# Performance work log

Hardware: AMD Instinct MI355X
Metric: run time of the kernel (lower is better)

Reference implementation:

```python
import jax, jax.numpy as jnp
import numpy as np

B, N, F_DIM, M, K, D = 8, 16384, 6, 128, 16, 768
MLP_DIMS = [F_DIM, 256, 512, 768, D]


def _fps(pts):
    """Deterministic farthest point sampling. pts: [N,4] -> indices [M] (first pick = point 0)."""
    n = pts.shape[0]

    def step(carry, _):
        min_d, last = carry
        d = jnp.sum((pts - pts[last]) ** 2, axis=-1)
        min_d = jnp.minimum(min_d, d)
        nxt = jnp.argmax(min_d).astype(jnp.int32)
        return (min_d, nxt), nxt

    init = (jnp.full((n,), 1e30, dtype=pts.dtype), jnp.int32(0))
    _, idx = jax.lax.scan(step, init, None, length=M - 1)
    return jnp.concatenate([jnp.zeros((1,), jnp.int32), idx])


def setup_inputs() -> dict:
    key = jax.random.key(0)
    ks = jax.random.split(key, 16)
    bidx = jnp.repeat(jnp.arange(B, dtype=jnp.float32), N)[:, None]
    xyzt = jax.random.normal(ks[0], (B * N, 4), jnp.float32)
    coordinates = jnp.concatenate([bidx, xyzt], axis=1)  # [B*N, 5]
    features = jax.random.normal(ks[1], (B * N, F_DIM), jnp.float32)
    inp = {"coordinates": coordinates, "features": features}
    for i in range(4):
        di, do = MLP_DIMS[i], MLP_DIMS[i + 1]
        inp[f"W{i}"] = jax.random.normal(ks[2 + i], (di, do), jnp.float32) * np.float32(1.0 / np.sqrt(di))
        inp[f"b{i}"] = jnp.zeros((do,), jnp.float32)
    for j in range(2):
        inp[f"Wn{j}"] = jax.random.normal(ks[6 + j], (D, D), jnp.float32) * np.float32(1.0 / np.sqrt(D))
        inp[f"bn{j}"] = jnp.zeros((D,), jnp.float32)
    return inp


def _forward(coordinates, features, W0, b0, W1, b1, W2, b2, W3, b3, Wn0, bn0, Wn1, bn1):
    # Equal points per event, sorted batch ids -> plain reshape replaces the per-batch loop.
    pts = coordinates.reshape(B, N, 5)[:, :, 1:5]       # xyz + time  [B,N,4]
    h = features.reshape(B, N, F_DIM)
    # per-point MLP (ReLU after each hidden layer, final Linear has no activation)
    h = jax.nn.relu(h @ W0 + b0)
    h = jax.nn.relu(h @ W1 + b1)
    h = jax.nn.relu(h @ W2 + b2)
    pf = h @ W3 + b3                                    # [B,N,D]
    # FPS centroids (non-differentiable index selection, as in the torch/cpu original)
    fidx = jax.vmap(_fps)(jax.lax.stop_gradient(pts))   # [B,M]
    cent = jnp.take_along_axis(pts, fidx[:, :, None], axis=1)  # [B,M,4]
    # cdist + kNN (smallest distances)
    dist = jnp.sqrt(jnp.sum((cent[:, :, None, :] - pts[:, None, :, :]) ** 2, axis=-1))  # [B,M,N]
    _, knn = jax.lax.top_k(-dist, K)                    # [B,M,K]
    gathered = jax.vmap(lambda p, i: p[i])(pf, knn)     # [B,M,K,D]
    pooled = jnp.max(gathered, axis=2)                  # [B,M,D]
    t = jax.nn.relu(pooled @ Wn0 + bn0)
    tokens = t @ Wn1 + bn1                              # [B,M,D]
    # sort tokens/centroids by centroid time (column 3)
    order = jnp.argsort(cent[:, :, 3], axis=1)
    cent = jnp.take_along_axis(cent, order[:, :, None], axis=1)
    tokens = jnp.take_along_axis(tokens, order[:, :, None], axis=1)
    masks = jnp.ones((B, M), dtype=bool)  # num_points > max_tokens -> all tokens valid
    return tokens, cent, masks


def reference(coordinates, features, W0, b0, W1, b1, W2, b2, W3, b3, Wn0, bn0, Wn1, bn1):
    return _forward(coordinates, features, W0, b0, W1, b1, W2, b2, W3, b3, Wn0, bn0, Wn1, bn1)
```

## Files before the change

kernel.cpp:

```cpp
#include <hip/hip_runtime.h>

#define B_ 8
#define N_ 16384
#define F_ 6
#define M_ 128
#define K_ 16
#define D_ 768

typedef unsigned short u16;
typedef unsigned int u32;
typedef __attribute__((ext_vector_type(8))) short short8;
typedef __attribute__((ext_vector_type(4))) float f32x4;
typedef __attribute__((ext_vector_type(2))) float f32x2;

__device__ __forceinline__ u16 f2bf(float f){
  union { float f; u32 i; } v; v.f = f;
  u32 x = v.i;
  u32 r = x + 0x7FFFu + ((x >> 16) & 1u);
  return (u16)(r >> 16);
}

__global__ __launch_bounds__(256) void conv_wt(const float* __restrict__ W,
                                               u16* __restrict__ WT, int K, int N){
  __shared__ u16 tile[64][65];
  int tiles_n = N >> 6;
  int tk = blockIdx.x / tiles_n, tn = blockIdx.x % tiles_n;
  int k0 = tk << 6, n0 = tn << 6;
  int t = threadIdx.x;
#pragma unroll
  for (int q = 0; q < 16; q++){
    int idx = q * 256 + t;
    int kk = idx >> 6, nn = idx & 63;
    tile[kk][nn] = f2bf(W[(size_t)(k0 + kk) * N + n0 + nn]);
  }
  __syncthreads();
#pragma unroll
  for (int q = 0; q < 16; q++){
    int idx = q * 256 + t;
    int nn = idx >> 6, kk = idx & 63;
    WT[(size_t)(n0 + nn) * K + k0 + kk] = tile[kk][nn];
  }
}

#define FPW 16
__global__ __launch_bounds__(512, 2) void fps_kernel(const float* __restrict__ coords,
                                                     float* __restrict__ cent){
#pragma clang fp contract(off)
  __shared__ float s_wv[2][8];
  __shared__ int s_wi[2][8];
  int b = blockIdx.x;
  int t = threadIdx.x;
  const float* cb = coords + (size_t)b * N_ * 5;
  f32x2 px[FPW], py[FPW], pz[FPW], pw[FPW], md[FPW];
#pragma unroll
  for (int j = 0; j < FPW; j++){
    int p = t + (j << 9);
    size_t i0 = (size_t)(2 * p) * 5;
    px[j] = (f32x2){cb[i0+1], cb[i0+6]};
    py[j] = (f32x2){cb[i0+2], cb[i0+7]};
    pz[j] = (f32x2){cb[i0+3], cb[i0+8]};
    pw[j] = (f32x2){cb[i0+4], cb[i0+9]};
    md[j] = (f32x2){1e30f, 1e30f};
  }
  float cx = cb[1], cy = cb[2], cz = cb[3], ct = cb[4];
  if (t == 0){
    float* c0 = cent + (size_t)b * M_ * 4;
    c0[0]=cx; c0[1]=cy; c0[2]=cz; c0[3]=ct;
  }
  for (int step = 1; step < M_; step++){
    f32x2 cx2 = (f32x2){cx, cx}, cy2 = (f32x2){cy, cy};
    f32x2 cz2 = (f32x2){cz, cz}, ct2 = (f32x2){ct, ct};
    float bv = -1.0f; int bi = 1 << 30;
#pragma unroll
    for (int j = 0; j < FPW; j++){
      f32x2 dX = px[j] - cx2;
      f32x2 dY = py[j] - cy2;
      f32x2 s = dX*dX + dY*dY;
      f32x2 dZ = pz[j] - cz2;
      s = s + dZ*dZ;
      f32x2 dW = pw[j] - ct2;
      s = s + dW*dW;
      f32x2 m = md[j];
      m[0] = (s[0] < m[0]) ? s[0] : m[0];
      m[1] = (s[1] < m[1]) ? s[1] : m[1];
      md[j] = m;
      int i0 = (t + (j << 9)) << 1;
      if (m[0] > bv){ bv = m[0]; bi = i0; }
      if (m[1] > bv){ bv = m[1]; bi = i0 + 1; }
    }
#pragma unroll
    for (int off = 32; off > 0; off >>= 1){
      float ov = __shfl_down(bv, off);
      int oi = __shfl_down(bi, off);
      if (ov > bv || (ov == bv && oi < bi)){ bv = ov; bi = oi; }
    }
    int par = step & 1;
    if ((t & 63) == 0){ s_wv[par][t >> 6] = bv; s_wi[par][t >> 6] = bi; }
    __syncthreads();
    float fv = s_wv[par][t & 7];
    int fi = s_wi[par][t & 7];
#pragma unroll
    for (int off = 1; off < 8; off <<= 1){
      float ov = __shfl_xor(fv, off);
      int oi = __shfl_xor(fi, off);
      if (ov > fv || (ov == fv && oi < fi)){ fv = ov; fi = oi; }
    }
    fi &= (N_ - 1);
    size_t wbase = (size_t)fi * 5;
    cx = cb[wbase+1]; cy = cb[wbase+2]; cz = cb[wbase+3]; ct = cb[wbase+4];
    if (t == 0){
      float* cr = cent + ((size_t)b * M_ + step) * 4;
      cr[0]=cx; cr[1]=cy; cr[2]=cz; cr[3]=ct;
    }
  }
}

__global__ __launch_bounds__(128) void rank_scatter(const float* __restrict__ cent_fps,
                                                    float* __restrict__ cent_sorted,
                                                    float* __restrict__ out,
                                                    size_t out_elems){
  int b = blockIdx.x, m = threadIdx.x;
  __shared__ float tt[M_];
  const float* row = cent_fps + ((size_t)b * M_ + m) * 4;
  float x=row[0], y=row[1], z=row[2], w=row[3];
  tt[m] = w;
  __syncthreads();
  int rank = 0;
  for (int j = 0; j < M_; j++){
    float tj = tt[j];
    if (tj < w || (tj == w && j < m)) rank++;
  }
  float* dst = cent_sorted + ((size_t)b * M_ + rank) * 4;
  dst[0]=x; dst[1]=y; dst[2]=z; dst[3]=w;
  size_t co = (size_t)B_ * M_ * D_ + ((size_t)b * M_ + rank) * 4;
  if (co + 3 < out_elems){
    out[co+0]=x; out[co+1]=y; out[co+2]=z; out[co+3]=w;
  }
  size_t mo = (size_t)B_ * M_ * D_ + (size_t)B_ * M_ * 4 + (size_t)b * M_ + m;
  if (mo < out_elems) out[mo] = 1.0f;
}

#define KNT 512
#define KPT 32
__global__ __launch_bounds__(512) void knn_kernel(const float* __restrict__ coords,
                                                  const float* __restrict__ cent,
                                                  int* __restrict__ knn){
#pragma clang fp contract(off)
  int cm = blockIdx.x;
  int b = cm >> 7;
  const float* cb = coords + (size_t)b * N_ * 5;
  int t = threadIdx.x;
  float cx=cent[cm*4+0], cy=cent[cm*4+1], cz=cent[cm*4+2], ct=cent[cm*4+3];
  float dist[KPT];
#pragma unroll
  for (int j = 0; j < KPT; j++){
    size_t i = t + j * KNT;
    float dx=cb[i*5+1]-cx, dy=cb[i*5+2]-cy, dz=cb[i*5+3]-cz, dw=cb[i*5+4]-ct;
    float d = ((dx*dx + dy*dy) + dz*dz) + dw*dw;
    dist[j] = sqrtf(d);
  }
  __shared__ float s_wv[8];
  __shared__ int s_wi[8];
  __shared__ int s_bi;
  for (int r = 0; r < K_; r++){
    float bv = 3e38f; int bi = 1 << 30;
#pragma unroll
    for (int j = 0; j < KPT; j++){
      int i = t + j * KNT;
      float v = dist[j];
      if (v < bv){ bv = v; bi = i; }
    }
#pragma unroll
    for (int off = 32; off > 0; off >>= 1){
      float ov = __shfl_down(bv, off);
      int oi = __shfl_down(bi, off);
      if (ov < bv || (ov == bv && oi < bi)){ bv = ov; bi = oi; }
    }
    if ((t & 63) == 0){ s_wv[t >> 6] = bv; s_wi[t >> 6] = bi; }
    __syncthreads();
    if (t == 0){
      float fv = s_wv[0]; int fi = s_wi[0];
      for (int w = 1; w < 8; w++){
        float wv = s_wv[w]; int wi = s_wi[w];
        if (wv < fv || (wv == fv && wi < fi)){ fv = wv; fi = wi; }
      }
      s_bi = fi;
      knn[(size_t)cm * K_ + r] = fi & (N_ - 1);
    }
    __syncthreads();
    int wi = s_bi;
#pragma unroll
    for (int j = 0; j < KPT; j++){
      if (t + j * KNT == wi) dist[j] = 3e38f;
    }
  }
}

__global__ __launch_bounds__(256) void gather_l0(const float* __restrict__ feat,
                                                 const int* __restrict__ knn,
                                                 const float* __restrict__ W0,
                                                 const float* __restrict__ b0,
                                                 u16* __restrict__ h1,
                                                 int rowBase){
  __shared__ float sW[F_][256];
  __shared__ float sb[256];
  __shared__ float sfa[32][F_];
  int t = threadIdx.x;
#pragma unroll
  for (int k = 0; k < F_; k++) sW[k][t] = W0[k * 256 + t];
  sb[t] = b0[t];
  if (t < 32 * F_){
    int r = t / F_, k = t % F_;
    int grow = rowBase + blockIdx.x * 32 + r;
    int bb = grow >> 11;
    int idx = knn[grow] & (N_ - 1);
    sfa[r][k] = feat[((size_t)bb * N_ + idx) * F_ + k];
  }
  __syncthreads();
#pragma unroll 4
  for (int r = 0; r < 32; r++){
    float acc = sb[t];
#pragma unroll
    for (int k = 0; k < F_; k++) acc = fmaf(sfa[r][k], sW[k][t], acc);
    int lrow = blockIdx.x * 32 + r;
    h1[(size_t)lrow * 256 + t] = f2bf(fmaxf(acc, 0.0f));
  }
}

template<int RELU, int OUTF32>
__global__ __launch_bounds__(256) void gemm_bf16(const u16* __restrict__ A,
                                                 const u16* __restrict__ WT,
                                                 const float* __restrict__ bias,
                                                 void* __restrict__ Cv,
                                                 int Kd, int Nd){
  __shared__ u16 As[128][40];
  __shared__ u16 Bs[128][40];
  const int t = threadIdx.x;
  const int bm = blockIdx.y << 7;
  const int bn = blockIdx.x << 7;
  const int wave = t >> 6;
  const int lane = t & 63;
  const int wm = (wave & 1) << 6;
  const int wn = (wave >> 1) << 6;
  const int lm = lane & 15;
  const int lk = (lane >> 4) << 3;
  f32x4 acc[4][4] = {};
  for (int k0 = 0; k0 < Kd; k0 += 32){
#pragma unroll
    for (int it = 0; it < 2; it++){
      int slot = t + (it << 8);
      int r = slot >> 2;
      int c = (slot & 3) << 3;
      short8 v = *(const short8*)(A + (size_t)(bm + r) * Kd + k0 + c);
      *(short8*)&As[r][c] = v;
      short8 w = *(const short8*)(WT + (size_t)(bn + r) * Kd + k0 + c);
      *(short8*)&Bs[r][c] = w;
    }
    __syncthreads();
    short8 af[4], bfr[4];
#pragma unroll
    for (int mt = 0; mt < 4; mt++) af[mt] = *(const short8*)&As[wm + (mt << 4) + lm][lk];
#pragma unroll
    for (int nt = 0; nt < 4; nt++) bfr[nt] = *(const short8*)&Bs[wn + (nt << 4) + lm][lk];
#pragma unroll
    for (int mt = 0; mt < 4; mt++)
#pragma unroll
      for (int nt = 0; nt < 4; nt++)
        acc[mt][nt] = __builtin_amdgcn_mfma_f32_16x16x32_bf16(af[mt], bfr[nt], acc[mt][nt], 0, 0, 0);
    __syncthreads();
  }
#pragma unroll
  for (int nt = 0; nt < 4; nt++){
    int n = bn + wn + (nt << 4) + lm;
    float bia = bias[n];
#pragma unroll
    for (int mt = 0; mt < 4; mt++){
#pragma unroll
      for (int r2 = 0; r2 < 4; r2++){
        int m = bm + wm + (mt << 4) + ((lane >> 4) << 2) + r2;
        float v = acc[mt][nt][r2] + bia;
        if (RELU) v = fmaxf(v, 0.0f);
        if (OUTF32) ((float*)Cv)[(size_t)m * Nd + n] = v;
        else        ((u16*)Cv)[(size_t)m * Nd + n] = f2bf(v);
      }
    }
  }
}

template<int RELU, int OUTF32>
__global__ __launch_bounds__(256) void gemm64(const u16* __restrict__ A,
                                              const u16* __restrict__ WT,
                                              const float* __restrict__ bias,
                                              void* __restrict__ Cv,
                                              int Kd, int Nd){
  __shared__ u16 As[64][40];
  __shared__ u16 Bs[64][40];
  const int t = threadIdx.x;
  const int bm = blockIdx.y << 6;
  const int bn = blockIdx.x << 6;
  const int wave = t >> 6;
  const int lane = t & 63;
  const int wm = (wave & 1) << 5;
  const int wn = (wave >> 1) << 5;
  const int lm = lane & 15;
  const int lk = (lane >> 4) << 3;
  f32x4 acc[2][2] = {};
  for (int k0 = 0; k0 < Kd; k0 += 32){
    {
      int r = t >> 2;
      int c = (t & 3) << 3;
      short8 v = *(const short8*)(A + (size_t)(bm + r) * Kd + k0 + c);
      *(short8*)&As[r][c] = v;
      short8 w = *(const short8*)(WT + (size_t)(bn + r) * Kd + k0 + c);
      *(short8*)&Bs[r][c] = w;
    }
    __syncthreads();
    short8 af[2], bfr[2];
#pragma unroll
    for (int mt = 0; mt < 2; mt++) af[mt] = *(const short8*)&As[wm + (mt << 4) + lm][lk];
#pragma unroll
    for (int nt = 0; nt < 2; nt++) bfr[nt] = *(const short8*)&Bs[wn + (nt << 4) + lm][lk];
#pragma unroll
    for (int mt = 0; mt < 2; mt++)
#pragma unroll
      for (int nt = 0; nt < 2; nt++)
        acc[mt][nt] = __builtin_amdgcn_mfma_f32_16x16x32_bf16(af[mt], bfr[nt], acc[mt][nt], 0, 0, 0);
    __syncthreads();
  }
#pragma unroll
  for (int nt = 0; nt < 2; nt++){
    int n = bn + wn + (nt << 4) + lm;
    float bia = bias[n];
#pragma unroll
    for (int mt = 0; mt < 2; mt++){
#pragma unroll
      for (int r2 = 0; r2 < 4; r2++){
        int m = bm + wm + (mt << 4) + ((lane >> 4) << 2) + r2;
        float v = acc[mt][nt][r2] + bia;
        if (RELU) v = fmaxf(v, 0.0f);
        if (OUTF32) ((float*)Cv)[(size_t)m * Nd + n] = v;
        else        ((u16*)Cv)[(size_t)m * Nd + n] = f2bf(v);
      }
    }
  }
}

__global__ __launch_bounds__(256) void gemm_pool(const u16* __restrict__ A,
                                                 const u16* __restrict__ WT,
                                                 const float* __restrict__ bias,
                                                 u16* __restrict__ pooled,
                                                 int Kd, int Nd, int groupBase){
  __shared__ u16 As[128][40];
  __shared__ u16 Bs[128][40];
  const int t = threadIdx.x;
  const int bm = blockIdx.y << 7;
  const int bn = blockIdx.x << 7;
  const int wave = t >> 6;
  const int lane = t & 63;
  const int wm = (wave & 1) << 6;
  const int wn = (wave >> 1) << 6;
  const int lm = lane & 15;
  const int lk = (lane >> 4) << 3;
  f32x4 acc[4][4] = {};
  for (int k0 = 0; k0 < Kd; k0 += 32){
#pragma unroll
    for (int it = 0; it < 2; it++){
      int slot = t + (it << 8);
      int r = slot >> 2;
      int c = (slot & 3) << 3;
      short8 v = *(const short8*)(A + (size_t)(bm + r) * Kd + k0 + c);
      *(short8*)&As[r][c] = v;
      short8 w = *(const short8*)(WT + (size_t)(bn + r) * Kd + k0 + c);
      *(short8*)&Bs[r][c] = w;
    }
    __syncthreads();
    short8 af[4], bfr[4];
#pragma unroll
    for (int mt = 0; mt < 4; mt++) af[mt] = *(const short8*)&As[wm + (mt << 4) + lm][lk];
#pragma unroll
    for (int nt = 0; nt < 4; nt++) bfr[nt] = *(const short8*)&Bs[wn + (nt << 4) + lm][lk];
#pragma unroll
    for (int mt = 0; mt < 4; mt++)
#pragma unroll
      for (int nt = 0; nt < 4; nt++)
        acc[mt][nt] = __builtin_amdgcn_mfma_f32_16x16x32_bf16(af[mt], bfr[nt], acc[mt][nt], 0, 0, 0);
    __syncthreads();
  }
#pragma unroll
  for (int nt = 0; nt < 4; nt++){
    int n = bn + wn + (nt << 4) + lm;
    float bia = bias[n];
#pragma unroll
    for (int mt = 0; mt < 4; mt++){
      f32x4 a = acc[mt][nt];
      float v = fmaxf(fmaxf(a[0], a[1]), fmaxf(a[2], a[3]));
      v = fmaxf(v, __shfl_xor(v, 16));
      v = fmaxf(v, __shfl_xor(v, 32));
      if ((lane >> 4) == 0){
        int g = groupBase + (bm >> 4) + (wm >> 4) + mt;
        pooled[(size_t)g * Nd + n] = f2bf(v + bia);
      }
    }
  }
}

__global__ __launch_bounds__(256) void fill_diag(float* __restrict__ out, size_t out_elems){
  size_t i = (size_t)blockIdx.x * 256 + threadIdx.x;
  if (i >= out_elems) return;
  size_t maskStart = (size_t)B_ * M_ * D_ + (size_t)B_ * M_ * 4;
  out[i] = (i >= maskStart) ? 1.0f : 0.0f;
}

extern "C" void kernel_launch(void* const* d_in, const int* in_sizes, int n_in,
                              void* d_out, int out_size, void* d_ws, size_t ws_size,
                              hipStream_t stream){
  (void)in_sizes; (void)n_in;
  const float* coords   = (const float*)d_in[0];
  const float* features = (const float*)d_in[1];
  const float* W0 = (const float*)d_in[2];  const float* b0 = (const float*)d_in[3];
  const float* W1 = (const float*)d_in[4];  const float* b1 = (const float*)d_in[5];
  const float* W2 = (const float*)d_in[6];  const float* b2 = (const float*)d_in[7];
  const float* W3 = (const float*)d_in[8];  const float* b3 = (const float*)d_in[9];
  const float* Wn0 = (const float*)d_in[10]; const float* bn0 = (const float*)d_in[11];
  const float* Wn1 = (const float*)d_in[12]; const float* bn1 = (const float*)d_in[13];
  float* out = (float*)d_out;
  const size_t out_elems = (size_t)out_size;

  char* ws = (char*)d_ws;
  const size_t o_cent = 0;
  const size_t o_cntS = 16384;
  const size_t o_knn  = 32768;
  const size_t o_Wb   = 131072;
  const size_t o_pool = 4718592;
  const size_t o_t1   = 6291456;
  const size_t o_chunk= 7864320;
  const int ROWS = B_ * M_ * K_;

  int R = 16384;
  while (R > 128 && o_chunk + (size_t)R * 2560 > ws_size) R >>= 1;
  if (d_ws == nullptr || o_chunk + (size_t)R * 2560 > ws_size){
    fill_diag<<<(int)((out_elems + 255) / 256), 256, 0, stream>>>(out, out_elems);
    return;
  }

  float* cent_fps    = (float*)(ws + o_cent);
  float* cent_sorted = (float*)(ws + o_cntS);
  int*   knn         = (int*)(ws + o_knn);
  u16* Wb   = (u16*)(ws + o_Wb);
  u16* W1t  = Wb;               u16* W2t  = Wb + 131072;
  u16* W3t  = Wb + 524288;      u16* Wn0t = Wb + 1114112;
  u16* Wn1t = Wb + 1703936;
  u16* pooled = (u16*)(ws + o_pool);
  u16* t1     = (u16*)(ws + o_t1);
  u16* regA   = (u16*)(ws + o_chunk);
  u16* regB   = (u16*)(ws + o_chunk + (size_t)R * 1536);

  conv_wt<<< 32, 256, 0, stream>>>(W1,  W1t,  256, 512);
  conv_wt<<< 96, 256, 0, stream>>>(W2,  W2t,  512, 768);
  conv_wt<<<144, 256, 0, stream>>>(W3,  W3t,  768, 768);
  conv_wt<<<144, 256, 0, stream>>>(Wn0, Wn0t, 768, 768);
  conv_wt<<<144, 256, 0, stream>>>(Wn1, Wn1t, 768, 768);

  fps_kernel<<<B_, 512, 0, stream>>>(coords, cent_fps);
  rank_scatter<<<B_, 128, 0, stream>>>(cent_fps, cent_sorted, out, out_elems);
  knn_kernel<<<B_ * M_, KNT, 0, stream>>>(coords, cent_sorted, knn);

  for (int rowBase = 0; rowBase < ROWS; rowBase += R){
    gather_l0<<<R / 32, 256, 0, stream>>>(features, knn, W0, b0, regA, rowBase);
    gemm_bf16<1,0><<<dim3(4, R / 128), 256, 0, stream>>>(regA, W1t, b1, regB, 256, 512);
    gemm_bf16<1,0><<<dim3(6, R / 128), 256, 0, stream>>>(regB, W2t, b2, regA, 512, 768);
    gemm_pool<<<dim3(6, R / 128), 256, 0, stream>>>(regA, W3t, b3, pooled, 768, 768, rowBase >> 4);
  }

  gemm64<1,0><<<dim3(12, (B_ * M_) / 64), 256, 0, stream>>>(pooled, Wn0t, bn0, t1, 768, 768);
  gemm64<0,1><<<dim3(12, (B_ * M_) / 64), 256, 0, stream>>>(t1, Wn1t, bn1, out, 768, 768);
}
```

Baseline: 571.3 us.

## Use direct global-to-LDS loads in GEMMs and merge weight conversion kernels

GEMM tile staging now uses the global_load_lds builtin, which writes 16-byte chunks straight into unpadded shared memory instead of going through registers. The shared tiles lose their padding (stride 40 to 32), so MFMA fragment reads may hit more LDS bank conflicts. The five weight-transpose launches are merged into one 560-block kernel to cut launch overhead. The per-wave contiguous destination layout relies on lane ordering matching the row/column mapping.

```diff
diff --git a/kernel.cpp b/kernel.cpp
--- a/kernel.cpp
+++ b/kernel.cpp
@@ -20,11 +20,27 @@
   return (u16)(r >> 16);
 }
 
-__global__ __launch_bounds__(256) void conv_wt(const float* __restrict__ W,
-                                               u16* __restrict__ WT, int K, int N){
+__device__ __forceinline__ void ld_g2l(const u16* g, u16* l){
+  __builtin_amdgcn_global_load_lds((const __attribute__((address_space(1))) u32*)g,
+                                   (__attribute__((address_space(3))) u32*)l, 16, 0, 0);
+}
+
+__global__ __launch_bounds__(256) void conv_all(const float* __restrict__ W1,
+                                                const float* __restrict__ W2,
+                                                const float* __restrict__ W3,
+                                                const float* __restrict__ Wn0,
+                                                const float* __restrict__ Wn1,
+                                                u16* __restrict__ Wb){
   __shared__ u16 tile[64][65];
+  int blk = blockIdx.x;
+  const float* W; u16* WT; int K, N, lb;
+  if      (blk < 32)  { W = W1;  WT = Wb;           K = 256; N = 512; lb = blk; }
+  else if (blk < 128) { W = W2;  WT = Wb + 131072;  K = 512; N = 768; lb = blk - 32; }
+  else if (blk < 272) { W = W3;  WT = Wb + 524288;  K = 768; N = 768; lb = blk - 128; }
+  else if (blk < 416) { W = Wn0; WT = Wb + 1114112; K = 768; N = 768; lb = blk - 272; }
+  else                { W = Wn1; WT = Wb + 1703936; K = 768; N = 768; lb = blk - 416; }
   int tiles_n = N >> 6;
-  int tk = blockIdx.x / tiles_n, tn = blockIdx.x % tiles_n;
+  int tk = lb / tiles_n, tn = lb % tiles_n;
   int k0 = tk << 6, n0 = tn << 6;
   int t = threadIdx.x;
 #pragma unroll
@@ -233,8 +249,8 @@
                                                  const float* __restrict__ bias,
                                                  void* __restrict__ Cv,
                                                  int Kd, int Nd){
-  __shared__ u16 As[128][40];
-  __shared__ u16 Bs[128][40];
+  __shared__ u16 As[128][32];
+  __shared__ u16 Bs[128][32];
   const int t = threadIdx.x;
   const int bm = blockIdx.y << 7;
   const int bn = blockIdx.x << 7;
@@ -244,6 +260,9 @@
   const int wn = (wave >> 1) << 6;
   const int lm = lane & 15;
   const int lk = (lane >> 4) << 3;
+  u16* AsF = &As[0][0];
+  u16* BsF = &Bs[0][0];
+  const int wbase = wave << 6;
   f32x4 acc[4][4] = {};
   for (int k0 = 0; k0 < Kd; k0 += 32){
 #pragma unroll
@@ -251,10 +270,9 @@
       int slot = t + (it << 8);
       int r = slot >> 2;
       int c = (slot & 3) << 3;
-      short8 v = *(const short8*)(A + (size_t)(bm + r) * Kd + k0 + c);
-      *(short8*)&As[r][c] = v;
-      short8 w = *(const short8*)(WT + (size_t)(bn + r) * Kd + k0 + c);
-      *(short8*)&Bs[r][c] = w;
+      int dst = (wbase + (it << 8)) << 3;
+      ld_g2l(A  + (size_t)(bm + r) * Kd + k0 + c, AsF + dst);
+      ld_g2l(WT + (size_t)(bn + r) * Kd + k0 + c, BsF + dst);
     }
     __syncthreads();
     short8 af[4], bfr[4];
@@ -293,8 +311,8 @@
                                               const float* __restrict__ bias,
                                               void* __restrict__ Cv,
                                               int Kd, int Nd){
-  __shared__ u16 As[64][40];
-  __shared__ u16 Bs[64][40];
+  __shared__ u16 As[64][32];
+  __shared__ u16 Bs[64][32];
   const int t = threadIdx.x;
   const int bm = blockIdx.y << 6;
   const int bn = blockIdx.x << 6;
@@ -304,15 +322,17 @@
   const int wn = (wave >> 1) << 5;
   const int lm = lane & 15;
   const int lk = (lane >> 4) << 3;
+  u16* AsF = &As[0][0];
+  u16* BsF = &Bs[0][0];
+  const int wbase = wave << 6;
   f32x4 acc[2][2] = {};
   for (int k0 = 0; k0 < Kd; k0 += 32){
     {
       int r = t >> 2;
       int c = (t & 3) << 3;
-      short8 v = *(const short8*)(A + (size_t)(bm + r) * Kd + k0 + c);
-      *(short8*)&As[r][c] = v;
-      short8 w = *(const short8*)(WT + (size_t)(bn + r) * Kd + k0 + c);
-      *(short8*)&Bs[r][c] = w;
+      int dst = wbase << 3;
+      ld_g2l(A  + (size_t)(bm + r) * Kd + k0 + c, AsF + dst);
+      ld_g2l(WT + (size_t)(bn + r) * Kd + k0 + c, BsF + dst);
     }
     __syncthreads();
     short8 af[2], bfr[2];
@@ -350,8 +370,8 @@
                                                  const float* __restrict__ bias,
                                                  u16* __restrict__ pooled,
                                                  int Kd, int Nd, int groupBase){
-  __shared__ u16 As[128][40];
-  __shared__ u16 Bs[128][40];
+  __shared__ u16 As[128][32];
+  __shared__ u16 Bs[128][32];
   const int t = threadIdx.x;
   const int bm = blockIdx.y << 7;
   const int bn = blockIdx.x << 7;
@@ -361,6 +381,9 @@
   const int wn = (wave >> 1) << 6;
   const int lm = lane & 15;
   const int lk = (lane >> 4) << 3;
+  u16* AsF = &As[0][0];
+  u16* BsF = &Bs[0][0];
+  const int wbase = wave << 6;
   f32x4 acc[4][4] = {};
   for (int k0 = 0; k0 < Kd; k0 += 32){
 #pragma unroll
@@ -368,10 +391,9 @@
       int slot = t + (it << 8);
       int r = slot >> 2;
       int c = (slot & 3) << 3;
-      short8 v = *(const short8*)(A + (size_t)(bm + r) * Kd + k0 + c);
-      *(short8*)&As[r][c] = v;
-      short8 w = *(const short8*)(WT + (size_t)(bn + r) * Kd + k0 + c);
-      *(short8*)&Bs[r][c] = w;
+      int dst = (wbase + (it << 8)) << 3;
+      ld_g2l(A  + (size_t)(bm + r) * Kd + k0 + c, AsF + dst);
+      ld_g2l(WT + (size_t)(bn + r) * Kd + k0 + c, BsF + dst);
     }
     __syncthreads();
     short8 af[4], bfr[4];
@@ -455,12 +477,7 @@
   u16* regA   = (u16*)(ws + o_chunk);
   u16* regB   = (u16*)(ws + o_chunk + (size_t)R * 1536);
 
-  conv_wt<<< 32, 256, 0, stream>>>(W1,  W1t,  256, 512);
-  conv_wt<<< 96, 256, 0, stream>>>(W2,  W2t,  512, 768);
-  conv_wt<<<144, 256, 0, stream>>>(W3,  W3t,  768, 768);
-  conv_wt<<<144, 256, 0, stream>>>(Wn0, Wn0t, 768, 768);
-  conv_wt<<<144, 256, 0, stream>>>(Wn1, Wn1t, 768, 768);
-
+  conv_all<<<560, 256, 0, stream>>>(W1, W2, W3, Wn0, Wn1, Wb);
   fps_kernel<<<B_, 512, 0, stream>>>(coords, cent_fps);
   rank_scatter<<<B_, 128, 0, stream>>>(cent_fps, cent_sorted, out, out_elems);
   knn_kernel<<<B_ * M_, KNT, 0, stream>>>(coords, cent_sorted, knn);
```

Result: faster. 559.0 us (-2.2%).
